# Kernel optimization log

Measured on AMD Instinct MI355X. Metric: run time of the kernel, lower is better.

## Reference

```python
import jax, jax.numpy as jnp
import numpy as np

B, N, DK = 16, 2048, 512

def setup_inputs() -> dict:
    key = jax.random.key(0)
    k1, k2, k3, k4 = jax.random.split(key, 4)
    return {
        'src_embedding': jax.random.normal(k1, (B, N, DK), dtype=jnp.float32),
        'target_embedding': jax.random.normal(k2, (B, N, DK), dtype=jnp.float32),
        'src': jax.random.normal(k3, (B, N, 3), dtype=jnp.float32),
        'target': jax.random.normal(k4, (B, N, 3), dtype=jnp.float32),
    }

def reference(src_embedding, target_embedding, src, target):
    d_k = src_embedding.shape[2]
    # attention-weighted soft correspondence: [B, N, M]
    scores = jnp.einsum('bnd,bmd->bnm', src_embedding, target_embedding)
    scores = jax.nn.softmax(scores / jnp.sqrt(jnp.asarray(d_k, scores.dtype)), axis=2)
    tgt_corr = jnp.einsum('bnm,bmc->bnc', scores, src)            # [B, N, 3]
    tgt_mean = jnp.mean(target, axis=1, keepdims=True)            # [B, 1, 3]
    corr_mean = jnp.mean(tgt_corr, axis=1, keepdims=True)         # [B, 1, 3]
    # cross-covariance H = (target - mu_t)^T @ (tgt_corr - mu_c): [B, 3, 3]
    H = jnp.einsum('bnc,bnd->bcd', target - tgt_mean, tgt_corr - corr_mean)
    U, S, Vh = jnp.linalg.svd(H)                                  # H = U diag(S) Vh
    det = jnp.linalg.det(jnp.matmul(U, Vh))                       # [B]
    # C = diag(1, 1, det) reflection fix; R = U @ C @ Vh
    diag = jnp.stack([jnp.ones_like(det), jnp.ones_like(det), det], axis=-1)  # [B, 3]
    R = jnp.matmul(U * diag[:, None, :], Vh)                      # [B, 3, 3]
    # t^T = mu_t^T - R @ mu_c^T, returned as [B, 1, 3]
    t = tgt_mean - jnp.einsum('bij,bkj->bki', R, corr_mean)
    return (R, t)
```

## Files before the change

kernel.cpp:

```cpp
#include <hip/hip_runtime.h>
#include <hip/hip_bf16.h>
#include <stdint.h>


#define B_  16
#define N_  2048
#define DK_ 512
#define SCALE 0.044194173824159216f

typedef __bf16 bf16x8 __attribute__((ext_vector_type(8)));
typedef float  f32x16 __attribute__((ext_vector_type(16)));
typedef float  f32x4  __attribute__((ext_vector_type(4)));

union BF8 { bf16x8 v; unsigned u[4]; };

__device__ inline unsigned pkbf(float a, float b) {
  unsigned r;
  asm("v_cvt_pk_bf16_f32 %0, %1, %2" : "=v"(r) : "v"(a), "v"(b));
  return r;
}

__device__ inline void gl_lds16(const void* g, void* l) {
  __builtin_amdgcn_global_load_lds(
      (const __attribute__((address_space(1))) unsigned int*)g,
      (__attribute__((address_space(3))) unsigned int*)l, 16, 0, 0);
}

__global__ __launch_bounds__(256)
void cvt_k_kernel(const float* __restrict__ in, uint4* __restrict__ out)
{
  const size_t total = (size_t)B_ * N_ * DK_ / 8;
  for (size_t i = (size_t)blockIdx.x * 256 + threadIdx.x; i < total;
       i += (size_t)gridDim.x * 256) {
    f32x4 a = ((const f32x4*)in)[2 * i];
    f32x4 c = ((const f32x4*)in)[2 * i + 1];
    uint4 w;
    w.x = pkbf(a[0], a[1]);
    w.y = pkbf(a[2], a[3]);
    w.z = pkbf(c[0], c[1]);
    w.w = pkbf(c[2], c[3]);
    out[i] = w;
  }
}

__global__ __launch_bounds__(256, 2)
void attn_stats_kernel(const float* __restrict__ Q,
                       const unsigned char* __restrict__ Kbf,
                       const float* __restrict__ Vsrc, float* __restrict__ part)
{
  __shared__ __align__(16) unsigned char s_k[2][32 * 1024];
  __shared__ __align__(16) float s_srcT[3 * 1024];

  const int L   = blockIdx.x;
  const int xcd = L & 7;
  const int kk  = L >> 3;
  const int b   = xcd + 8 * (kk & 1);
  const int ms  = (kk >> 1) & 1;
  const int nb  = kk >> 2;

  const int tid  = threadIdx.x;
  const int lane = tid & 63;
  const int wid  = tid >> 6;
  const int row  = lane & 31;
  const int hi   = lane >> 5;

  const int mchunk0 = ms * 1024;

  {
    const float* vp = Vsrc + ((size_t)b * N_ + mchunk0) * 3;
    for (int idx = tid; idx < 3072; idx += 256) {
      int m = idx / 3, c = idx - 3 * m;
      s_srcT[c * 1024 + m] = vp[idx];
    }
  }

  const int qglob = nb * 128 + wid * 32 + row;
  BF8 qf[32];
  {
    const f32x4* qp = (const f32x4*)(Q + ((size_t)b * N_ + qglob) * DK_);
    #pragma unroll
    for (int t = 0; t < 32; ++t) {
      f32x4 f0 = qp[t * 4 + hi * 2];
      f32x4 f1 = qp[t * 4 + hi * 2 + 1];
      qf[t].u[0] = pkbf(f0[0], f0[1]);
      qf[t].u[1] = pkbf(f0[2], f0[3]);
      qf[t].u[2] = pkbf(f1[0], f1[1]);
      qf[t].u[3] = pkbf(f1[2], f1[3]);
    }
  }

  const unsigned char* kbase = Kbf + ((size_t)b * N_ + mchunk0) * (DK_ * 2);

  #define STAGE(bb, t)                                                       \
    { _Pragma("unroll")                                                      \
      for (int j = 0; j < 8; ++j) {                                          \
        const int r_ = wid * 8 + j;                                          \
        gl_lds16(kbase + (((size_t)(t) * 32 + r_) << 10)                     \
                       + (unsigned)((lane ^ r_) << 4),                       \
                 &s_k[bb][r_ << 10]);                                        \
      } }

  float lsum = 0.f, a0 = 0.f, a1 = 0.f, a2 = 0.f;

  const unsigned kread_base = (unsigned)(row * 1024);
  const unsigned kread_xor  = (unsigned)(row << 4);

  STAGE(0, 0)
  __syncthreads();

  for (int tile = 0; tile < 32; ++tile) {
    const int cur = tile & 1;
    if (tile + 1 < 32) STAGE(cur ^ 1, tile + 1)

    const unsigned char* bp = &s_k[cur][0];
    f32x16 sc0, sc1;
    #pragma unroll
    for (int i = 0; i < 16; ++i) { sc0[i] = 0.f; sc1[i] = 0.f; }
    __builtin_amdgcn_s_setprio(1);
    #pragma unroll
    for (int t = 0; t < 32; t += 2) {
      BF8 kf0, kf1;
      kf0.v = *(const bf16x8*)(bp + kread_base +
                (((unsigned)(t * 32 + hi * 16)) ^ kread_xor));
      sc0 = __builtin_amdgcn_mfma_f32_32x32x16_bf16(kf0.v, qf[t].v, sc0, 0, 0, 0);
      kf1.v = *(const bf16x8*)(bp + kread_base +
                (((unsigned)((t + 1) * 32 + hi * 16)) ^ kread_xor));
      sc1 = __builtin_amdgcn_mfma_f32_32x32x16_bf16(kf1.v, qf[t + 1].v, sc1, 0, 0, 0);
    }
    __builtin_amdgcn_s_setprio(0);

    #pragma unroll
    for (int j = 0; j < 4; ++j) {
      const int mrun = tile * 32 + j * 8 + hi * 4;
      f32x4 s0 = *(const f32x4*)&s_srcT[mrun];
      f32x4 s1 = *(const f32x4*)&s_srcT[1024 + mrun];
      f32x4 s2 = *(const f32x4*)&s_srcT[2048 + mrun];
      #pragma unroll
      for (int i2 = 0; i2 < 4; ++i2) {
        float w = __expf((sc0[j * 4 + i2] + sc1[j * 4 + i2]) * SCALE);
        lsum += w;
        a0 += w * s0[i2];
        a1 += w * s1[i2];
        a2 += w * s2[i2];
      }
    }

    __syncthreads();
  }
  #undef STAGE

  a0   += __shfl_xor(a0, 32);
  a1   += __shfl_xor(a1, 32);
  a2   += __shfl_xor(a2, 32);
  lsum += __shfl_xor(lsum, 32);

  if (hi == 0) {
    f32x4 o; o[0] = a0; o[1] = a1; o[2] = a2; o[3] = lsum;
    *(f32x4*)(part + (((size_t)ms * B_ + b) * N_ + qglob) * 4) = o;
  }
}

__global__ __launch_bounds__(512, 2)
void attn_stats_f32_kernel(const float* __restrict__ Q, const float* __restrict__ K,
                           const float* __restrict__ Vsrc, float* __restrict__ part)
{
  __shared__ __align__(16) unsigned char s_k[32 * 1024];
  __shared__ __align__(16) float s_srcT[3 * 1024];

  const int L   = blockIdx.x;
  const int xcd = L & 7;
  const int kk  = L >> 3;
  const int b   = xcd + 8 * (kk & 1);
  const int ms  = (kk >> 1) & 1;
  const int nb  = kk >> 2;

  const int tid  = threadIdx.x;
  const int lane = tid & 63;
  const int wid  = tid >> 6;
  const int row  = lane & 31;
  const int hi   = lane >> 5;

  const int mchunk0 = ms * 1024;

  {
    const float* vp = Vsrc + ((size_t)b * N_ + mchunk0) * 3;
    for (int idx = tid; idx < 3072; idx += 512) {
      int m = idx / 3, c = idx - 3 * m;
      s_srcT[c * 1024 + m] = vp[idx];
    }
  }

  const int qglob = nb * 256 + wid * 32 + row;
  BF8 qf[32];
  {
    const f32x4* qp = (const f32x4*)(Q + ((size_t)b * N_ + qglob) * DK_);
    #pragma unroll
    for (int t = 0; t < 32; ++t) {
      f32x4 f0 = qp[t * 4 + hi * 2];
      f32x4 f1 = qp[t * 4 + hi * 2 + 1];
      qf[t].u[0] = pkbf(f0[0], f0[1]);
      qf[t].u[1] = pkbf(f0[2], f0[3]);
      qf[t].u[2] = pkbf(f1[0], f1[1]);
      qf[t].u[3] = pkbf(f1[2], f1[3]);
    }
  }

  const f32x4* kg = (const f32x4*)(K + ((size_t)b * N_ + mchunk0) * DK_);

  float lsum = 0.f, a0 = 0.f, a1 = 0.f, a2 = 0.f;

  f32x4 stg[8];
  #pragma unroll
  for (int i = 0; i < 8; ++i) stg[i] = kg[i * 512 + tid];

  const unsigned kread_base = (unsigned)(row * 1024);
  const unsigned kread_xor  = (unsigned)(row << 4);

  for (int tile = 0; tile < 32; ++tile) {
    __syncthreads();
    #pragma unroll
    for (int i = 0; i < 8; ++i) {
      int idx  = i * 512 + tid;
      int r    = idx >> 7;
      int colb = (idx & 127) * 8;
      unsigned addr = (unsigned)(r * 1024) + ((unsigned)colb ^ ((unsigned)(r << 4)));
      uint2 w2;
      w2.x = pkbf(stg[i][0], stg[i][1]);
      w2.y = pkbf(stg[i][2], stg[i][3]);
      *(uint2*)(s_k + addr) = w2;
    }
    __syncthreads();
    if (tile + 1 < 32) {
      const f32x4* kt = kg + (size_t)(tile + 1) * 4096;
      #pragma unroll
      for (int i = 0; i < 8; ++i) stg[i] = kt[i * 512 + tid];
    }
    f32x16 sc0, sc1;
    #pragma unroll
    for (int i = 0; i < 16; ++i) { sc0[i] = 0.f; sc1[i] = 0.f; }
    __builtin_amdgcn_s_setprio(1);
    #pragma unroll
    for (int t = 0; t < 32; t += 2) {
      BF8 kf0, kf1;
      kf0.v = *(const bf16x8*)(s_k + kread_base +
                (((unsigned)(t * 32 + hi * 16)) ^ kread_xor));
      sc0 = __builtin_amdgcn_mfma_f32_32x32x16_bf16(kf0.v, qf[t].v, sc0, 0, 0, 0);
      kf1.v = *(const bf16x8*)(s_k + kread_base +
                (((unsigned)((t + 1) * 32 + hi * 16)) ^ kread_xor));
      sc1 = __builtin_amdgcn_mfma_f32_32x32x16_bf16(kf1.v, qf[t + 1].v, sc1, 0, 0, 0);
    }
    __builtin_amdgcn_s_setprio(0);
    #pragma unroll
    for (int j = 0; j < 4; ++j) {
      const int mrun = tile * 32 + j * 8 + hi * 4;
      f32x4 s0 = *(const f32x4*)&s_srcT[mrun];
      f32x4 s1 = *(const f32x4*)&s_srcT[1024 + mrun];
      f32x4 s2 = *(const f32x4*)&s_srcT[2048 + mrun];
      #pragma unroll
      for (int i2 = 0; i2 < 4; ++i2) {
        float w = __expf((sc0[j * 4 + i2] + sc1[j * 4 + i2]) * SCALE);
        lsum += w;
        a0 += w * s0[i2];
        a1 += w * s1[i2];
        a2 += w * s2[i2];
      }
    }
  }

  a0   += __shfl_xor(a0, 32);
  a1   += __shfl_xor(a1, 32);
  a2   += __shfl_xor(a2, 32);
  lsum += __shfl_xor(lsum, 32);

  if (hi == 0) {
    f32x4 o; o[0] = a0; o[1] = a1; o[2] = a2; o[3] = lsum;
    *(f32x4*)(part + (((size_t)ms * B_ + b) * N_ + qglob) * 4) = o;
  }
}

__global__ void reduce_kernel(const float* __restrict__ part,
                              const float* __restrict__ tgt,
                              float* __restrict__ ws2)
{
  const int b = blockIdx.x, tid = threadIdx.x;
  float s[15];
  #pragma unroll
  for (int j = 0; j < 15; ++j) s[j] = 0.f;

  for (int n = tid; n < N_; n += 256) {
    f32x4 p0 = *(const f32x4*)(part + (((size_t)0 * B_ + b) * N_ + n) * 4);
    f32x4 p1 = *(const f32x4*)(part + (((size_t)1 * B_ + b) * N_ + n) * 4);
    float inv = 1.0f / (p0[3] + p1[3]);
    float c0 = (p0[0] + p1[0]) * inv;
    float c1 = (p0[1] + p1[1]) * inv;
    float c2 = (p0[2] + p1[2]) * inv;
    const float* tp = tgt + ((size_t)b * N_ + n) * 3;
    float t0 = tp[0], t1 = tp[1], t2 = tp[2];
    s[0] += t0;  s[1] += t1;  s[2] += t2;
    s[3] += c0;  s[4] += c1;  s[5] += c2;
    s[6] += t0 * c0;  s[7]  += t0 * c1;  s[8]  += t0 * c2;
    s[9] += t1 * c0;  s[10] += t1 * c1;  s[11] += t1 * c2;
    s[12] += t2 * c0; s[13] += t2 * c1;  s[14] += t2 * c2;
  }
  #pragma unroll
  for (int j = 0; j < 15; ++j) {
    #pragma unroll
    for (int off = 32; off > 0; off >>= 1) s[j] += __shfl_xor(s[j], off);
  }
  __shared__ float red[4][15];
  int lane = tid & 63, w = tid >> 6;
  if (lane == 0) {
    #pragma unroll
    for (int j = 0; j < 15; ++j) red[w][j] = s[j];
  }
  __syncthreads();
  if (tid < 15)
    ws2[b * 16 + tid] = red[0][tid] + red[1][tid] + red[2][tid] + red[3][tid];
}

__device__ inline void jrot(double A[3][3], double V[3][3], int p, int q) {
  double apq = A[p][q];
  if (fabs(apq) < 1e-300) return;
  double tau = (A[q][q] - A[p][p]) / (2.0 * apq);
  double tt = (tau >= 0.0) ? 1.0 / (tau + sqrt(1.0 + tau * tau))
                           : 1.0 / (tau - sqrt(1.0 + tau * tau));
  double c = 1.0 / sqrt(1.0 + tt * tt), sn = tt * c;
  for (int k = 0; k < 3; ++k) {
    double akp = A[k][p], akq = A[k][q];
    A[k][p] = c * akp - sn * akq;
    A[k][q] = sn * akp + c * akq;
  }
  for (int k = 0; k < 3; ++k) {
    double apk = A[p][k], aqk = A[q][k];
    A[p][k] = c * apk - sn * aqk;
    A[q][k] = sn * apk + c * aqk;
  }
  for (int k = 0; k < 3; ++k) {
    double vkp = V[k][p], vkq = V[k][q];
    V[k][p] = c * vkp - sn * vkq;
    V[k][q] = sn * vkp + c * vkq;
  }
}

__global__ void svd_kernel(const float* __restrict__ ws2, float* __restrict__ out)
{
  const int b = threadIdx.x;
  if (b >= B_) return;
  const float* s = ws2 + b * 16;
  const double invN = 1.0 / (double)N_;
  double stv[3] = {s[0], s[1], s[2]};
  double scv[3] = {s[3], s[4], s[5]};
  double H[3][3];
  for (int c = 0; c < 3; ++c)
    for (int d = 0; d < 3; ++d)
      H[c][d] = (double)s[6 + c * 3 + d] - stv[c] * scv[d] * invN;

  double A[3][3], V[3][3] = {{1,0,0},{0,1,0},{0,0,1}};
  for (int i = 0; i < 3; ++i)
    for (int j = 0; j < 3; ++j) {
      double acc = 0.0;
      for (int c = 0; c < 3; ++c) acc += H[c][i] * H[c][j];
      A[i][j] = acc;
    }
  for (int sw = 0; sw < 15; ++sw) { jrot(A,V,0,1); jrot(A,V,0,2); jrot(A,V,1,2); }

  double e[3] = {A[0][0], A[1][1], A[2][2]};
  double vc[3][3];
  for (int k = 0; k < 3; ++k)
    for (int i = 0; i < 3; ++i) vc[k][i] = V[i][k];
  for (int a2 = 0; a2 < 2; ++a2)
    for (int b2 = 0; b2 < 2 - a2; ++b2)
      if (e[b2] < e[b2 + 1]) {
        double te = e[b2]; e[b2] = e[b2 + 1]; e[b2 + 1] = te;
        for (int i = 0; i < 3; ++i) {
          double tv = vc[b2][i]; vc[b2][i] = vc[b2 + 1][i]; vc[b2 + 1][i] = tv;
        }
      }

  double u1[3], u2[3], u3[3];
  for (int i = 0; i < 3; ++i)
    u1[i] = H[i][0]*vc[0][0] + H[i][1]*vc[0][1] + H[i][2]*vc[0][2];
  double n1 = sqrt(u1[0]*u1[0] + u1[1]*u1[1] + u1[2]*u1[2]);
  n1 = fmax(n1, 1e-300);
  for (int i = 0; i < 3; ++i) u1[i] /= n1;
  for (int i = 0; i < 3; ++i)
    u2[i] = H[i][0]*vc[1][0] + H[i][1]*vc[1][1] + H[i][2]*vc[1][2];
  double d12 = u1[0]*u2[0] + u1[1]*u2[1] + u1[2]*u2[2];
  for (int i = 0; i < 3; ++i) u2[i] -= d12 * u1[i];
  double n2 = sqrt(u2[0]*u2[0] + u2[1]*u2[1] + u2[2]*u2[2]);
  n2 = fmax(n2, 1e-300);
  for (int i = 0; i < 3; ++i) u2[i] /= n2;
  u3[0] = u1[1]*u2[2] - u1[2]*u2[1];
  u3[1] = u1[2]*u2[0] - u1[0]*u2[2];
  u3[2] = u1[0]*u2[1] - u1[1]*u2[0];

  double detV = vc[0][0]*(vc[1][1]*vc[2][2] - vc[1][2]*vc[2][1])
              - vc[0][1]*(vc[1][0]*vc[2][2] - vc[1][2]*vc[2][0])
              + vc[0][2]*(vc[1][0]*vc[2][1] - vc[1][1]*vc[2][0]);

  double R[3][3];
  for (int i = 0; i < 3; ++i)
    for (int j = 0; j < 3; ++j)
      R[i][j] = u1[i]*vc[0][j] + u2[i]*vc[1][j] + detV * u3[i]*vc[2][j];

  for (int i = 0; i < 3; ++i)
    for (int j = 0; j < 3; ++j)
      out[b * 9 + i * 3 + j] = (float)R[i][j];

  double muc[3] = {scv[0]*invN, scv[1]*invN, scv[2]*invN};
  for (int i = 0; i < 3; ++i) {
    double ti = stv[i]*invN - (R[i][0]*muc[0] + R[i][1]*muc[1] + R[i][2]*muc[2]);
    out[B_ * 9 + b * 3 + i] = (float)ti;
  }
}

extern "C" void kernel_launch(void* const* d_in, const int* in_sizes, int n_in,
                              void* d_out, int out_size, void* d_ws, size_t ws_size,
                              hipStream_t stream)
{
  const float* srcE = (const float*)d_in[0];
  const float* tgtE = (const float*)d_in[1];
  const float* srcP = (const float*)d_in[2];
  const float* tgtP = (const float*)d_in[3];
  float* out = (float*)d_out;

  const size_t kbf_bytes   = (size_t)B_ * N_ * DK_ * 2;
  const size_t part_floats = (size_t)2 * B_ * N_ * 4;

  if (ws_size >= kbf_bytes + part_floats * 4 + 1024) {
    unsigned char* kbf = (unsigned char*)d_ws;
    float* part = (float*)(kbf + kbf_bytes);
    float* ws2  = part + part_floats;
    cvt_k_kernel<<<dim3(2048), dim3(256), 0, stream>>>(tgtE, (uint4*)kbf);
    attn_stats_kernel<<<dim3(512), dim3(256), 0, stream>>>(srcE, kbf, srcP, part);
    reduce_kernel<<<dim3(B_), dim3(256), 0, stream>>>(part, tgtP, ws2);
    svd_kernel<<<dim3(1), dim3(64), 0, stream>>>(ws2, out);
  } else {
    float* part = (float*)d_ws;
    float* ws2  = part + part_floats;
    attn_stats_f32_kernel<<<dim3(256), dim3(512), 0, stream>>>(srcE, tgtE, srcP, part);
    reduce_kernel<<<dim3(B_), dim3(256), 0, stream>>>(part, tgtP, ws2);
    svd_kernel<<<dim3(1), dim3(64), 0, stream>>>(ws2, out);
  }
}
```

Baseline: 145.7 us.

## Process two query tiles per wave to reuse K fragments across MFMAs

Each wave now computes scores for 64 query rows (two 32-row tiles) against every staged K tile, sharing each LDS-loaded K fragment between two MFMAs. The grid is halved, so K is staged and read from LDS half as often per query. The cost is doubled Q fragments and accumulators in registers, which forces launch bounds to one block per CU and reduces occupancy and latency hiding.

```diff
diff --git a/kernel.cpp b/kernel.cpp
--- a/kernel.cpp
+++ b/kernel.cpp
@@ -43,7 +43,7 @@
   }
 }
 
-__global__ __launch_bounds__(256, 2)
+__global__ __launch_bounds__(256, 1)
 void attn_stats_kernel(const float* __restrict__ Q,
                        const unsigned char* __restrict__ Kbf,
                        const float* __restrict__ Vsrc, float* __restrict__ part)
@@ -74,18 +74,26 @@
     }
   }
 
-  const int qglob = nb * 128 + wid * 32 + row;
-  BF8 qf[32];
+  const int qglobA = nb * 256 + wid * 64 + row;
+  const int qglobB = qglobA + 32;
+  BF8 qfA[32], qfB[32];
   {
-    const f32x4* qp = (const f32x4*)(Q + ((size_t)b * N_ + qglob) * DK_);
+    const f32x4* qpA = (const f32x4*)(Q + ((size_t)b * N_ + qglobA) * DK_);
+    const f32x4* qpB = (const f32x4*)(Q + ((size_t)b * N_ + qglobB) * DK_);
     #pragma unroll
     for (int t = 0; t < 32; ++t) {
-      f32x4 f0 = qp[t * 4 + hi * 2];
-      f32x4 f1 = qp[t * 4 + hi * 2 + 1];
-      qf[t].u[0] = pkbf(f0[0], f0[1]);
-      qf[t].u[1] = pkbf(f0[2], f0[3]);
-      qf[t].u[2] = pkbf(f1[0], f1[1]);
-      qf[t].u[3] = pkbf(f1[2], f1[3]);
+      f32x4 f0 = qpA[t * 4 + hi * 2];
+      f32x4 f1 = qpA[t * 4 + hi * 2 + 1];
+      qfA[t].u[0] = pkbf(f0[0], f0[1]);
+      qfA[t].u[1] = pkbf(f0[2], f0[3]);
+      qfA[t].u[2] = pkbf(f1[0], f1[1]);
+      qfA[t].u[3] = pkbf(f1[2], f1[3]);
+      f32x4 g0 = qpB[t * 4 + hi * 2];
+      f32x4 g1 = qpB[t * 4 + hi * 2 + 1];
+      qfB[t].u[0] = pkbf(g0[0], g0[1]);
+      qfB[t].u[1] = pkbf(g0[2], g0[3]);
+      qfB[t].u[2] = pkbf(g1[0], g1[1]);
+      qfB[t].u[3] = pkbf(g1[2], g1[3]);
     }
   }
 
@@ -100,7 +108,8 @@
                  &s_k[bb][r_ << 10]);                                        \
       } }
 
-  float lsum = 0.f, a0 = 0.f, a1 = 0.f, a2 = 0.f;
+  float lsumA = 0.f, a0A = 0.f, a1A = 0.f, a2A = 0.f;
+  float lsumB = 0.f, a0B = 0.f, a1B = 0.f, a2B = 0.f;
 
   const unsigned kread_base = (unsigned)(row * 1024);
   const unsigned kread_xor  = (unsigned)(row << 4);
@@ -113,19 +122,23 @@
     if (tile + 1 < 32) STAGE(cur ^ 1, tile + 1)
 
     const unsigned char* bp = &s_k[cur][0];
-    f32x16 sc0, sc1;
-    #pragma unroll
-    for (int i = 0; i < 16; ++i) { sc0[i] = 0.f; sc1[i] = 0.f; }
+    f32x16 scA0, scA1, scB0, scB1;
+    #pragma unroll
+    for (int i = 0; i < 16; ++i) {
+      scA0[i] = 0.f; scA1[i] = 0.f; scB0[i] = 0.f; scB1[i] = 0.f;
+    }
     __builtin_amdgcn_s_setprio(1);
     #pragma unroll
     for (int t = 0; t < 32; t += 2) {
       BF8 kf0, kf1;
       kf0.v = *(const bf16x8*)(bp + kread_base +
                 (((unsigned)(t * 32 + hi * 16)) ^ kread_xor));
-      sc0 = __builtin_amdgcn_mfma_f32_32x32x16_bf16(kf0.v, qf[t].v, sc0, 0, 0, 0);
+      scA0 = __builtin_amdgcn_mfma_f32_32x32x16_bf16(kf0.v, qfA[t].v, scA0, 0, 0, 0);
+      scB0 = __builtin_amdgcn_mfma_f32_32x32x16_bf16(kf0.v, qfB[t].v, scB0, 0, 0, 0);
       kf1.v = *(const bf16x8*)(bp + kread_base +
                 (((unsigned)((t + 1) * 32 + hi * 16)) ^ kread_xor));
-      sc1 = __builtin_amdgcn_mfma_f32_32x32x16_bf16(kf1.v, qf[t + 1].v, sc1, 0, 0, 0);
+      scA1 = __builtin_amdgcn_mfma_f32_32x32x16_bf16(kf1.v, qfA[t + 1].v, scA1, 0, 0, 0);
+      scB1 = __builtin_amdgcn_mfma_f32_32x32x16_bf16(kf1.v, qfB[t + 1].v, scB1, 0, 0, 0);
     }
     __builtin_amdgcn_s_setprio(0);
 
@@ -137,11 +150,16 @@
       f32x4 s2 = *(const f32x4*)&s_srcT[2048 + mrun];
       #pragma unroll
       for (int i2 = 0; i2 < 4; ++i2) {
-        float w = __expf((sc0[j * 4 + i2] + sc1[j * 4 + i2]) * SCALE);
-        lsum += w;
-        a0 += w * s0[i2];
-        a1 += w * s1[i2];
-        a2 += w * s2[i2];
+        float wA = __expf((scA0[j * 4 + i2] + scA1[j * 4 + i2]) * SCALE);
+        lsumA += wA;
+        a0A += wA * s0[i2];
+        a1A += wA * s1[i2];
+        a2A += wA * s2[i2];
+        float wB = __expf((scB0[j * 4 + i2] + scB1[j * 4 + i2]) * SCALE);
+        lsumB += wB;
+        a0B += wB * s0[i2];
+        a1B += wB * s1[i2];
+        a2B += wB * s2[i2];
       }
     }
 
@@ -149,14 +167,20 @@
   }
   #undef STAGE
 
-  a0   += __shfl_xor(a0, 32);
-  a1   += __shfl_xor(a1, 32);
-  a2   += __shfl_xor(a2, 32);
-  lsum += __shfl_xor(lsum, 32);
+  a0A   += __shfl_xor(a0A, 32);
+  a1A   += __shfl_xor(a1A, 32);
+  a2A   += __shfl_xor(a2A, 32);
+  lsumA += __shfl_xor(lsumA, 32);
+  a0B   += __shfl_xor(a0B, 32);
+  a1B   += __shfl_xor(a1B, 32);
+  a2B   += __shfl_xor(a2B, 32);
+  lsumB += __shfl_xor(lsumB, 32);
 
   if (hi == 0) {
-    f32x4 o; o[0] = a0; o[1] = a1; o[2] = a2; o[3] = lsum;
-    *(f32x4*)(part + (((size_t)ms * B_ + b) * N_ + qglob) * 4) = o;
+    f32x4 oA; oA[0] = a0A; oA[1] = a1A; oA[2] = a2A; oA[3] = lsumA;
+    *(f32x4*)(part + (((size_t)ms * B_ + b) * N_ + qglobA) * 4) = oA;
+    f32x4 oB; oB[0] = a0B; oB[1] = a1B; oB[2] = a2B; oB[3] = lsumB;
+    *(f32x4*)(part + (((size_t)ms * B_ + b) * N_ + qglobB) * 4) = oB;
   }
 }
 
@@ -432,7 +456,7 @@
     float* part = (float*)(kbf + kbf_bytes);
     float* ws2  = part + part_floats;
     cvt_k_kernel<<<dim3(2048), dim3(256), 0, stream>>>(tgtE, (uint4*)kbf);
-    attn_stats_kernel<<<dim3(512), dim3(256), 0, stream>>>(srcE, kbf, srcP, part);
+    attn_stats_kernel<<<dim3(256), dim3(256), 0, stream>>>(srcE, kbf, srcP, part);
     reduce_kernel<<<dim3(B_), dim3(256), 0, stream>>>(part, tgtP, ws2);
     svd_kernel<<<dim3(1), dim3(64), 0, stream>>>(ws2, out);
   } else {
```

New measurement: 157.4 us. +8.1%, slower.

## Split key dimension into four slices and single-buffer LDS for higher occupancy

Applied to the files above, without the earlier changes.

The attention-stats kernel now splits the M (key) range into four 512-row slices instead of two, doubling the grid to 1024 blocks. LDS staging drops from a double buffer to a single 32 KB buffer and the launch bound allows four blocks per CU. The aim is more resident waves to hide load latency, replacing in-block prefetch overlap with cross-block overlap. The cost is an explicit load wait before every tile, more partial sums written, and a reduce kernel that now reads four partial slices.

```diff
diff --git a/kernel.cpp b/kernel.cpp
--- a/kernel.cpp
+++ b/kernel.cpp
@@ -43,20 +43,20 @@
   }
 }
 
-__global__ __launch_bounds__(256, 2)
+__global__ __launch_bounds__(256, 4)
 void attn_stats_kernel(const float* __restrict__ Q,
                        const unsigned char* __restrict__ Kbf,
                        const float* __restrict__ Vsrc, float* __restrict__ part)
 {
-  __shared__ __align__(16) unsigned char s_k[2][32 * 1024];
-  __shared__ __align__(16) float s_srcT[3 * 1024];
+  __shared__ __align__(16) unsigned char s_k[32 * 1024];
+  __shared__ __align__(16) float s_srcT[3 * 512];
 
   const int L   = blockIdx.x;
   const int xcd = L & 7;
   const int kk  = L >> 3;
   const int b   = xcd + 8 * (kk & 1);
-  const int ms  = (kk >> 1) & 1;
-  const int nb  = kk >> 2;
+  const int ms  = (kk >> 1) & 3;
+  const int nb  = kk >> 3;
 
   const int tid  = threadIdx.x;
   const int lane = tid & 63;
@@ -64,13 +64,13 @@
   const int row  = lane & 31;
   const int hi   = lane >> 5;
 
-  const int mchunk0 = ms * 1024;
+  const int mchunk0 = ms * 512;
 
   {
     const float* vp = Vsrc + ((size_t)b * N_ + mchunk0) * 3;
-    for (int idx = tid; idx < 3072; idx += 256) {
+    for (int idx = tid; idx < 1536; idx += 256) {
       int m = idx / 3, c = idx - 3 * m;
-      s_srcT[c * 1024 + m] = vp[idx];
+      s_srcT[c * 512 + m] = vp[idx];
     }
   }
 
@@ -91,13 +91,13 @@
 
   const unsigned char* kbase = Kbf + ((size_t)b * N_ + mchunk0) * (DK_ * 2);
 
-  #define STAGE(bb, t)                                                       \
+  #define STAGE(t)                                                           \
     { _Pragma("unroll")                                                      \
       for (int j = 0; j < 8; ++j) {                                          \
         const int r_ = wid * 8 + j;                                          \
         gl_lds16(kbase + (((size_t)(t) * 32 + r_) << 10)                     \
                        + (unsigned)((lane ^ r_) << 4),                       \
-                 &s_k[bb][r_ << 10]);                                        \
+                 s_k + (r_ << 10));                                          \
       } }
 
   float lsum = 0.f, a0 = 0.f, a1 = 0.f, a2 = 0.f;
@@ -105,14 +105,11 @@
   const unsigned kread_base = (unsigned)(row * 1024);
   const unsigned kread_xor  = (unsigned)(row << 4);
 
-  STAGE(0, 0)
-  __syncthreads();
-
-  for (int tile = 0; tile < 32; ++tile) {
-    const int cur = tile & 1;
-    if (tile + 1 < 32) STAGE(cur ^ 1, tile + 1)
-
-    const unsigned char* bp = &s_k[cur][0];
+  for (int tile = 0; tile < 16; ++tile) {
+    STAGE(tile)
+    asm volatile("s_waitcnt vmcnt(0)" ::: "memory");
+    __syncthreads();
+
     f32x16 sc0, sc1;
     #pragma unroll
     for (int i = 0; i < 16; ++i) { sc0[i] = 0.f; sc1[i] = 0.f; }
@@ -120,15 +117,136 @@
     #pragma unroll
     for (int t = 0; t < 32; t += 2) {
       BF8 kf0, kf1;
-      kf0.v = *(const bf16x8*)(bp + kread_base +
+      kf0.v = *(const bf16x8*)(s_k + kread_base +
                 (((unsigned)(t * 32 + hi * 16)) ^ kread_xor));
       sc0 = __builtin_amdgcn_mfma_f32_32x32x16_bf16(kf0.v, qf[t].v, sc0, 0, 0, 0);
-      kf1.v = *(const bf16x8*)(bp + kread_base +
+      kf1.v = *(const bf16x8*)(s_k + kread_base +
                 (((unsigned)((t + 1) * 32 + hi * 16)) ^ kread_xor));
       sc1 = __builtin_amdgcn_mfma_f32_32x32x16_bf16(kf1.v, qf[t + 1].v, sc1, 0, 0, 0);
     }
     __builtin_amdgcn_s_setprio(0);
 
+    #pragma unroll
+    for (int j = 0; j < 4; ++j) {
+      const int mrun = tile * 32 + j * 8 + hi * 4;
+      f32x4 s0 = *(const f32x4*)&s_srcT[mrun];
+      f32x4 s1 = *(const f32x4*)&s_srcT[512 + mrun];
+      f32x4 s2 = *(const f32x4*)&s_srcT[1024 + mrun];
+      #pragma unroll
+      for (int i2 = 0; i2 < 4; ++i2) {
+        float w = __expf((sc0[j * 4 + i2] + sc1[j * 4 + i2]) * SCALE);
+        lsum += w;
+        a0 += w * s0[i2];
+        a1 += w * s1[i2];
+        a2 += w * s2[i2];
+      }
+    }
+
+    __syncthreads();
+  }
+  #undef STAGE
+
+  a0   += __shfl_xor(a0, 32);
+  a1   += __shfl_xor(a1, 32);
+  a2   += __shfl_xor(a2, 32);
+  lsum += __shfl_xor(lsum, 32);
+
+  if (hi == 0) {
+    f32x4 o; o[0] = a0; o[1] = a1; o[2] = a2; o[3] = lsum;
+    *(f32x4*)(part + (((size_t)ms * B_ + b) * N_ + qglob) * 4) = o;
+  }
+}
+
+__global__ __launch_bounds__(512, 2)
+void attn_stats_f32_kernel(const float* __restrict__ Q, const float* __restrict__ K,
+                           const float* __restrict__ Vsrc, float* __restrict__ part)
+{
+  __shared__ __align__(16) unsigned char s_k[32 * 1024];
+  __shared__ __align__(16) float s_srcT[3 * 1024];
+
+  const int L   = blockIdx.x;
+  const int xcd = L & 7;
+  const int kk  = L >> 3;
+  const int b   = xcd + 8 * (kk & 1);
+  const int ms  = (kk >> 1) & 1;
+  const int nb  = kk >> 2;
+
+  const int tid  = threadIdx.x;
+  const int lane = tid & 63;
+  const int wid  = tid >> 6;
+  const int row  = lane & 31;
+  const int hi   = lane >> 5;
+
+  const int mchunk0 = ms * 1024;
+
+  {
+    const float* vp = Vsrc + ((size_t)b * N_ + mchunk0) * 3;
+    for (int idx = tid; idx < 3072; idx += 512) {
+      int m = idx / 3, c = idx - 3 * m;
+      s_srcT[c * 1024 + m] = vp[idx];
+    }
+  }
+
+  const int qglob = nb * 256 + wid * 32 + row;
+  BF8 qf[32];
+  {
+    const f32x4* qp = (const f32x4*)(Q + ((size_t)b * N_ + qglob) * DK_);
+    #pragma unroll
+    for (int t = 0; t < 32; ++t) {
+      f32x4 f0 = qp[t * 4 + hi * 2];
+      f32x4 f1 = qp[t * 4 + hi * 2 + 1];
+      qf[t].u[0] = pkbf(f0[0], f0[1]);
+      qf[t].u[1] = pkbf(f0[2], f0[3]);
+      qf[t].u[2] = pkbf(f1[0], f1[1]);
+      qf[t].u[3] = pkbf(f1[2], f1[3]);
+    }
+  }
+
+  const f32x4* kg = (const f32x4*)(K + ((size_t)b * N_ + mchunk0) * DK_);
+
+  float lsum = 0.f, a0 = 0.f, a1 = 0.f, a2 = 0.f;
+
+  f32x4 stg[8];
+  #pragma unroll
+  for (int i = 0; i < 8; ++i) stg[i] = kg[i * 512 + tid];
+
+  const unsigned kread_base = (unsigned)(row * 1024);
+  const unsigned kread_xor  = (unsigned)(row << 4);
+
+  for (int tile = 0; tile < 32; ++tile) {
+    __syncthreads();
+    #pragma unroll
+    for (int i = 0; i < 8; ++i) {
+      int idx  = i * 512 + tid;
+      int r    = idx >> 7;
+      int colb = (idx & 127) * 8;
+      unsigned addr = (unsigned)(r * 1024) + ((unsigned)colb ^ ((unsigned)(r << 4)));
+      uint2 w2;
+      w2.x = pkbf(stg[i][0], stg[i][1]);
+      w2.y = pkbf(stg[i][2], stg[i][3]);
+      *(uint2*)(s_k + addr) = w2;
+    }
+    __syncthreads();
+    if (tile + 1 < 32) {
+      const f32x4* kt = kg + (size_t)(tile + 1) * 4096;
+      #pragma unroll
+      for (int i = 0; i < 8; ++i) stg[i] = kt[i * 512 + tid];
+    }
+    f32x16 sc0, sc1;
+    #pragma unroll
+    for (int i = 0; i < 16; ++i) { sc0[i] = 0.f; sc1[i] = 0.f; }
+    __builtin_amdgcn_s_setprio(1);
+    #pragma unroll
+    for (int t = 0; t < 32; t += 2) {
+      BF8 kf0, kf1;
+      kf0.v = *(const bf16x8*)(s_k + kread_base +
+                (((unsigned)(t * 32 + hi * 16)) ^ kread_xor));
+      sc0 = __builtin_amdgcn_mfma_f32_32x32x16_bf16(kf0.v, qf[t].v, sc0, 0, 0, 0);
+      kf1.v = *(const bf16x8*)(s_k + kread_base +
+                (((unsigned)((t + 1) * 32 + hi * 16)) ^ kread_xor));
+      sc1 = __builtin_amdgcn_mfma_f32_32x32x16_bf16(kf1.v, qf[t + 1].v, sc1, 0, 0, 0);
+    }
+    __builtin_amdgcn_s_setprio(0);
     #pragma unroll
     for (int j = 0; j < 4; ++j) {
       const int mrun = tile * 32 + j * 8 + hi * 4;
@@ -144,10 +262,7 @@
         a2 += w * s2[i2];
       }
     }
-
-    __syncthreads();
-  }
-  #undef STAGE
+  }
 
   a0   += __shfl_xor(a0, 32);
   a1   += __shfl_xor(a1, 32);
@@ -160,127 +275,9 @@
   }
 }
 
-__global__ __launch_bounds__(512, 2)
-void attn_stats_f32_kernel(const float* __restrict__ Q, const float* __restrict__ K,
-                           const float* __restrict__ Vsrc, float* __restrict__ part)
-{
-  __shared__ __align__(16) unsigned char s_k[32 * 1024];
-  __shared__ __align__(16) float s_srcT[3 * 1024];
-
-  const int L   = blockIdx.x;
-  const int xcd = L & 7;
-  const int kk  = L >> 3;
-  const int b   = xcd + 8 * (kk & 1);
-  const int ms  = (kk >> 1) & 1;
-  const int nb  = kk >> 2;
-
-  const int tid  = threadIdx.x;
-  const int lane = tid & 63;
-  const int wid  = tid >> 6;
-  const int row  = lane & 31;
-  const int hi   = lane >> 5;
-
-  const int mchunk0 = ms * 1024;
-
-  {
-    const float* vp = Vsrc + ((size_t)b * N_ + mchunk0) * 3;
-    for (int idx = tid; idx < 3072; idx += 512) {
-      int m = idx / 3, c = idx - 3 * m;
-      s_srcT[c * 1024 + m] = vp[idx];
-    }
-  }
-
-  const int qglob = nb * 256 + wid * 32 + row;
-  BF8 qf[32];
-  {
-    const f32x4* qp = (const f32x4*)(Q + ((size_t)b * N_ + qglob) * DK_);
-    #pragma unroll
-    for (int t = 0; t < 32; ++t) {
-      f32x4 f0 = qp[t * 4 + hi * 2];
-      f32x4 f1 = qp[t * 4 + hi * 2 + 1];
-      qf[t].u[0] = pkbf(f0[0], f0[1]);
-      qf[t].u[1] = pkbf(f0[2], f0[3]);
-      qf[t].u[2] = pkbf(f1[0], f1[1]);
-      qf[t].u[3] = pkbf(f1[2], f1[3]);
-    }
-  }
-
-  const f32x4* kg = (const f32x4*)(K + ((size_t)b * N_ + mchunk0) * DK_);
-
-  float lsum = 0.f, a0 = 0.f, a1 = 0.f, a2 = 0.f;
-
-  f32x4 stg[8];
-  #pragma unroll
-  for (int i = 0; i < 8; ++i) stg[i] = kg[i * 512 + tid];
-
-  const unsigned kread_base = (unsigned)(row * 1024);
-  const unsigned kread_xor  = (unsigned)(row << 4);
-
-  for (int tile = 0; tile < 32; ++tile) {
-    __syncthreads();
-    #pragma unroll
-    for (int i = 0; i < 8; ++i) {
-      int idx  = i * 512 + tid;
-      int r    = idx >> 7;
-      int colb = (idx & 127) * 8;
-      unsigned addr = (unsigned)(r * 1024) + ((unsigned)colb ^ ((unsigned)(r << 4)));
-      uint2 w2;
-      w2.x = pkbf(stg[i][0], stg[i][1]);
-      w2.y = pkbf(stg[i][2], stg[i][3]);
-      *(uint2*)(s_k + addr) = w2;
-    }
-    __syncthreads();
-    if (tile + 1 < 32) {
-      const f32x4* kt = kg + (size_t)(tile + 1) * 4096;
-      #pragma unroll
-      for (int i = 0; i < 8; ++i) stg[i] = kt[i * 512 + tid];
-    }
-    f32x16 sc0, sc1;
-    #pragma unroll
-    for (int i = 0; i < 16; ++i) { sc0[i] = 0.f; sc1[i] = 0.f; }
-    __builtin_amdgcn_s_setprio(1);
-    #pragma unroll
-    for (int t = 0; t < 32; t += 2) {
-      BF8 kf0, kf1;
-      kf0.v = *(const bf16x8*)(s_k + kread_base +
-                (((unsigned)(t * 32 + hi * 16)) ^ kread_xor));
-      sc0 = __builtin_amdgcn_mfma_f32_32x32x16_bf16(kf0.v, qf[t].v, sc0, 0, 0, 0);
-      kf1.v = *(const bf16x8*)(s_k + kread_base +
-                (((unsigned)((t + 1) * 32 + hi * 16)) ^ kread_xor));
-      sc1 = __builtin_amdgcn_mfma_f32_32x32x16_bf16(kf1.v, qf[t + 1].v, sc1, 0, 0, 0);
-    }
-    __builtin_amdgcn_s_setprio(0);
-    #pragma unroll
-    for (int j = 0; j < 4; ++j) {
-      const int mrun = tile * 32 + j * 8 + hi * 4;
-      f32x4 s0 = *(const f32x4*)&s_srcT[mrun];
-      f32x4 s1 = *(const f32x4*)&s_srcT[1024 + mrun];
-      f32x4 s2 = *(const f32x4*)&s_srcT[2048 + mrun];
-      #pragma unroll
-      for (int i2 = 0; i2 < 4; ++i2) {
-        float w = __expf((sc0[j * 4 + i2] + sc1[j * 4 + i2]) * SCALE);
-        lsum += w;
-        a0 += w * s0[i2];
-        a1 += w * s1[i2];
-        a2 += w * s2[i2];
-      }
-    }
-  }
-
-  a0   += __shfl_xor(a0, 32);
-  a1   += __shfl_xor(a1, 32);
-  a2   += __shfl_xor(a2, 32);
-  lsum += __shfl_xor(lsum, 32);
-
-  if (hi == 0) {
-    f32x4 o; o[0] = a0; o[1] = a1; o[2] = a2; o[3] = lsum;
-    *(f32x4*)(part + (((size_t)ms * B_ + b) * N_ + qglob) * 4) = o;
-  }
-}
-
 __global__ void reduce_kernel(const float* __restrict__ part,
                               const float* __restrict__ tgt,
-                              float* __restrict__ ws2)
+                              float* __restrict__ ws2, int nslice)
 {
   const int b = blockIdx.x, tid = threadIdx.x;
   float s[15];
@@ -290,10 +287,20 @@
   for (int n = tid; n < N_; n += 256) {
     f32x4 p0 = *(const f32x4*)(part + (((size_t)0 * B_ + b) * N_ + n) * 4);
     f32x4 p1 = *(const f32x4*)(part + (((size_t)1 * B_ + b) * N_ + n) * 4);
-    float inv = 1.0f / (p0[3] + p1[3]);
-    float c0 = (p0[0] + p1[0]) * inv;
-    float c1 = (p0[1] + p1[1]) * inv;
-    float c2 = (p0[2] + p1[2]) * inv;
+    float l  = p0[3] + p1[3];
+    float c0 = p0[0] + p1[0];
+    float c1 = p0[1] + p1[1];
+    float c2 = p0[2] + p1[2];
+    if (nslice == 4) {
+      f32x4 p2 = *(const f32x4*)(part + (((size_t)2 * B_ + b) * N_ + n) * 4);
+      f32x4 p3 = *(const f32x4*)(part + (((size_t)3 * B_ + b) * N_ + n) * 4);
+      l  += p2[3] + p3[3];
+      c0 += p2[0] + p3[0];
+      c1 += p2[1] + p3[1];
+      c2 += p2[2] + p3[2];
+    }
+    float inv = 1.0f / l;
+    c0 *= inv; c1 *= inv; c2 *= inv;
     const float* tp = tgt + ((size_t)b * N_ + n) * 3;
     float t0 = tp[0], t1 = tp[1], t2 = tp[2];
     s[0] += t0;  s[1] += t1;  s[2] += t2;
@@ -425,21 +432,21 @@
   float* out = (float*)d_out;
 
   const size_t kbf_bytes   = (size_t)B_ * N_ * DK_ * 2;
-  const size_t part_floats = (size_t)2 * B_ * N_ * 4;
+  const size_t part_floats = (size_t)4 * B_ * N_ * 4;
 
   if (ws_size >= kbf_bytes + part_floats * 4 + 1024) {
     unsigned char* kbf = (unsigned char*)d_ws;
     float* part = (float*)(kbf + kbf_bytes);
     float* ws2  = part + part_floats;
     cvt_k_kernel<<<dim3(2048), dim3(256), 0, stream>>>(tgtE, (uint4*)kbf);
-    attn_stats_kernel<<<dim3(512), dim3(256), 0, stream>>>(srcE, kbf, srcP, part);
-    reduce_kernel<<<dim3(B_), dim3(256), 0, stream>>>(part, tgtP, ws2);
+    attn_stats_kernel<<<dim3(1024), dim3(256), 0, stream>>>(srcE, kbf, srcP, part);
+    reduce_kernel<<<dim3(B_), dim3(256), 0, stream>>>(part, tgtP, ws2, 4);
     svd_kernel<<<dim3(1), dim3(64), 0, stream>>>(ws2, out);
   } else {
     float* part = (float*)d_ws;
-    float* ws2  = part + part_floats;
+    float* ws2  = part + (size_t)2 * B_ * N_ * 4;
     attn_stats_f32_kernel<<<dim3(256), dim3(512), 0, stream>>>(srcE, tgtE, srcP, part);
-    reduce_kernel<<<dim3(B_), dim3(256), 0, stream>>>(part, tgtP, ws2);
+    reduce_kernel<<<dim3(B_), dim3(256), 0, stream>>>(part, tgtP, ws2, 2);
     svd_kernel<<<dim3(1), dim3(64), 0, stream>>>(ws2, out);
   }
 }
```

After: 423.4 us. +190.7%, slower.
